# Optimization experiments

Hardware: AMD Instinct MI355X
Metric: run time of the kernel (lower is better)

The kernel has to match this reference:

```python
import jax, jax.numpy as jnp
import numpy as np
import math

B, S, E, H, D = 2, 2048, 1024, 16, 64  # batch, seq, embed, heads, head_dim


def setup_inputs() -> dict:
    key = jax.random.key(0)
    ks = jax.random.split(key, 10)
    scale = 1.0 / math.sqrt(D)
    return {
        "query": jax.random.normal(ks[0], (B, S, E), jnp.float32),
        "key": jax.random.normal(ks[1], (B, S, E), jnp.float32),
        "value": jax.random.normal(ks[2], (B, S, E), jnp.float32),
        "mask": jax.random.randint(ks[3], (1, 1, S, S), 0, 2, jnp.int32),
        # nn.Linear(single_dim, single_dim) weights (out,in) and biases
        "Wq": jax.random.uniform(ks[4], (D, D), jnp.float32, -scale, scale),
        "bq": jax.random.uniform(ks[5], (D,), jnp.float32, -scale, scale),
        "Wk": jax.random.uniform(ks[6], (D, D), jnp.float32, -scale, scale),
        "bk": jax.random.uniform(ks[7], (D,), jnp.float32, -scale, scale),
        "Wv": jax.random.uniform(ks[8], (D, D), jnp.float32, -scale, scale),
        "bv": jax.random.uniform(ks[9], (D,), jnp.float32, -scale, scale),
    }


def reference(query, key, value, mask, Wq, bq, Wk, bk, Wv, bv):
    b, sq, _ = query.shape
    sk = key.shape[1]
    # (b, s, E) -> (b, H, s, D)
    q = query.reshape(b, sq, H, D).transpose(0, 2, 1, 3)
    k = key.reshape(b, sk, H, D).transpose(0, 2, 1, 3)
    v = value.reshape(b, sk, H, D).transpose(0, 2, 1, 3)
    # per-head shared Linear on last dim: x @ W^T + b
    q = jnp.einsum('bhsd,ed->bhse', q, Wq) + bq
    k = jnp.einsum('bhsd,ed->bhse', k, Wk) + bk
    v = jnp.einsum('bhsd,ed->bhse', v, Wv) + bv
    scores = jnp.einsum('bhqd,bhkd->bhqk', q, k) / math.sqrt(D)
    scores = jnp.where(mask == 0, jnp.float32(-1e20), scores)
    attn = jax.nn.softmax(scores, axis=-1)
    out = jnp.einsum('bhqk,bhkd->bhqd', attn, v)
    return out.transpose(0, 2, 1, 3).reshape(b, sq, H * D)
```

## Files before the change

### kernel.cpp

```cpp
#include <hip/hip_runtime.h>

#define S_LEN 2048
#define E_DIM 1024
#define NH 16
#define HD 64
#define NT (S_LEN / 64)
#define SCALE_L2E 0.18033688011112042f

typedef __bf16 bf16;
typedef __attribute__((ext_vector_type(4))) bf16 bf16x4;
typedef __attribute__((ext_vector_type(8))) bf16 bf16x8;
typedef __attribute__((ext_vector_type(4))) float f32x4;
typedef unsigned long long u64;
typedef unsigned int u32;

#define MFMA(a, b, c) __builtin_amdgcn_mfma_f32_16x16x32_bf16((a), (b), (c), 0, 0, 0)

__device__ __forceinline__ bf16x8 cvt8(f32x4 a, f32x4 b) {
  bf16x8 r;
  r[0] = (bf16)a[0]; r[1] = (bf16)a[1]; r[2] = (bf16)a[2]; r[3] = (bf16)a[3];
  r[4] = (bf16)b[0]; r[5] = (bf16)b[1]; r[6] = (bf16)b[2]; r[7] = (bf16)b[3];
  return r;
}

__device__ __forceinline__ bf16x8 load_cvt_frag(const float* p) {
  f32x4 a = *(const f32x4*)(p);
  f32x4 b = *(const f32x4*)(p + 16);
  return cvt8(a, b);
}

__global__ __launch_bounds__(256) void kvproj_k(
    const float* __restrict__ Kin, const float* __restrict__ Vin,
    const float* __restrict__ Wk, const float* __restrict__ bk,
    const float* __restrict__ Wv, const float* __restrict__ bv,
    const int* __restrict__ mask,
    bf16* __restrict__ KpF, bf16* __restrict__ VpF, u64* __restrict__ bits) {
  const int xcd = blockIdx.x & 7;
  const int idx = blockIdx.x >> 3;
  const int bh = xcd * 4 + (idx >> 5);
  const int sblk = idx & 31;
  const int h = bh & (NH - 1);
  const int b = bh >> 4;
  const int lane = threadIdx.x & 63;
  const int wave = threadIdx.x >> 6;
  const int g = lane >> 4;
  const int c16 = lane & 15;
  const int sbase = sblk * 64 + wave * 16;
  const int srow = sbase + c16;

  const float* xk = Kin + ((size_t)b * S_LEN + srow) * E_DIM + h * HD;
  const float* xv = Vin + ((size_t)b * S_LEN + srow) * E_DIM + h * HD;
  bf16x8 xkf[2], xvf[2];
#pragma unroll
  for (int c = 0; c < 2; ++c) {
    xkf[c] = load_cvt_frag(xk + 32 * c + 4 * g);
    xvf[c] = load_cvt_frag(xv + 32 * c + 4 * g);
  }

#pragma unroll
  for (int nt = 0; nt < 4; ++nt) {
    const float* wr = Wk + (16 * nt + c16) * HD + 4 * g;
    f32x4 acc = {0.f, 0.f, 0.f, 0.f};
    acc = MFMA(xkf[0], load_cvt_frag(wr), acc);
    acc = MFMA(xkf[1], load_cvt_frag(wr + 32), acc);
    const float bias = bk[16 * nt + c16];
    const size_t fidx = (((size_t)bh * 32 + sblk) * 4 + wave) * 2 + (nt >> 1);
    const int e = (c16 & 3) + 4 * (nt & 1);
#pragma unroll
    for (int r = 0; r < 4; ++r) {
      const int lane_p = (c16 >> 2) * 16 + 4 * g + r;
      KpF[fidx * 512 + lane_p * 8 + e] = (bf16)(acc[r] + bias);
    }
  }
#pragma unroll
  for (int nt = 0; nt < 4; ++nt) {
    const float* wr = Wv + (16 * nt + c16) * HD + 4 * g;
    f32x4 acc = {0.f, 0.f, 0.f, 0.f};
    acc = MFMA(load_cvt_frag(wr), xvf[0], acc);
    acc = MFMA(load_cvt_frag(wr + 32), xvf[1], acc);
    const size_t fidx = (((size_t)bh * 32 + sblk) * 4 + nt) * 2 + (wave >> 1);
    const int e = (c16 & 3) + 4 * (wave & 1);
#pragma unroll
    for (int r = 0; r < 4; ++r) {
      const int dout = 16 * nt + 4 * g + r;
      const int lane_p = (c16 >> 2) * 16 + 4 * g + r;
      VpF[fidx * 512 + lane_p * 8 + e] = (bf16)(acc[r] + bv[dout]);
    }
  }

  const int wbase = blockIdx.x * 64 + wave * 16;
  int mv[16];
#pragma unroll
  for (int i = 0; i < 16; ++i) mv[i] = mask[(size_t)(wbase + i) * 64 + lane];
#pragma unroll
  for (int i = 0; i < 16; ++i) {
    const u64 bb = __ballot(mv[i] != 0);
    const int w = wbase + i;
    if (lane == 0) bits[(size_t)(w & 31) * S_LEN + (w >> 5)] = bb;
  }
}

__global__ __launch_bounds__(512) void attn_k(
    const float* __restrict__ Qin, const float* __restrict__ Wq, const float* __restrict__ bq,
    const bf16* __restrict__ KpF, const bf16* __restrict__ VpF,
    const u64* __restrict__ mbits, float* __restrict__ out) {
  const int xcd = blockIdx.x & 7;
  const int idx = blockIdx.x >> 3;
  const int bh = xcd * 4 + (idx >> 4);
  const int qc = idx & 15;
  const int h = bh & (NH - 1);
  const int b = bh >> 4;
  const int lane = threadIdx.x & 63;
  const int wave = threadIdx.x >> 6;
  const int g = lane >> 4;
  const int c16 = lane & 15;
  const int qrow = qc * 128 + wave * 16 + c16;

  __shared__ __align__(16) bf16 lds_kv[3][16 * 512];

  const float* xq = Qin + ((size_t)b * S_LEN + qrow) * E_DIM + h * HD;
  bf16x8 xqf[2];
#pragma unroll
  for (int c = 0; c < 2; ++c) xqf[c] = load_cvt_frag(xq + 32 * c + 4 * g);
  f32x4 qt[4];
#pragma unroll
  for (int t = 0; t < 4; ++t) {
    const float* wr = Wq + (16 * t + c16) * HD + 4 * g;
    f32x4 acc = {0.f, 0.f, 0.f, 0.f};
    acc = MFMA(load_cvt_frag(wr), xqf[0], acc);
    acc = MFMA(load_cvt_frag(wr + 32), xqf[1], acc);
#pragma unroll
    for (int r = 0; r < 4; ++r) acc[r] = (acc[r] + bq[16 * t + 4 * g + r]) * SCALE_L2E;
    qt[t] = acc;
  }
  bf16x8 qfrag0 = cvt8(qt[0], qt[1]);
  bf16x8 qfrag1 = cvt8(qt[2], qt[3]);

  bf16x8 ones;
#pragma unroll
  for (int i = 0; i < 8; ++i) ones[i] = (bf16)1.0f;

  const bf16* ktile = KpF + ((size_t)bh * 32) * 4096;
  const bf16* vtile = VpF + ((size_t)bh * 32) * 4096;
  const u64* mrowT = mbits + qrow;

  f32x4 o[4] = {};
  f32x4 o5 = {};

#define STAGE(BUF, T)                                                              \
  {                                                                                \
    const bf16* ks_ = ktile + (size_t)(T) * 4096 + wave * 512 + lane * 8;          \
    const bf16* vs_ = vtile + (size_t)(T) * 4096 + wave * 512 + lane * 8;          \
    __builtin_amdgcn_global_load_lds(                                              \
        (const __attribute__((address_space(1))) u32*)ks_,                         \
        (__attribute__((address_space(3))) u32*)((BUF) + wave * 512), 16, 0, 0);   \
    __builtin_amdgcn_global_load_lds(                                              \
        (const __attribute__((address_space(1))) u32*)vs_,                         \
        (__attribute__((address_space(3))) u32*)((BUF) + 4096 + wave * 512), 16, 0, 0); \
  }

  bf16* b0 = &lds_kv[0][0];
  bf16* b1 = &lds_kv[1][0];
  bf16* b2 = &lds_kv[2][0];

  u64 mca, mcb;

  STAGE(b0, 0)
  STAGE(b1, 1)
  mca = mrowT[0];
  mcb = mrowT[S_LEN];
  asm volatile("s_waitcnt vmcnt(4)" ::: "memory");
  asm volatile("s_barrier" ::: "memory");

#define ITER(BUF, NXT, MREG, T)                                                   \
  {                                                                               \
    const u64 mw_ = MREG;                                                         \
    const bool more_ = (T) + 2 < NT;                                              \
    if (more_) {                                                                  \
      MREG = mrowT[(size_t)((T) + 2) * S_LEN];                                    \
      STAGE(NXT, (T) + 2)                                                         \
    }                                                                             \
    bf16x8 kf[8], vfr[8];                                                         \
    _Pragma("unroll") for (int f = 0; f < 8; ++f)                                 \
        kf[f] = *(const bf16x8*)((BUF) + f * 512 + lane * 8);                     \
    f32x4 st[4];                                                                  \
    __builtin_amdgcn_s_setprio(1);                                                \
    _Pragma("unroll") for (int ks = 0; ks < 4; ++ks) {                            \
      f32x4 acc = {0.f, 0.f, 0.f, 0.f};                                           \
      acc = MFMA(kf[2 * ks], qfrag0, acc);                                        \
      acc = MFMA(kf[2 * ks + 1], qfrag1, acc);                                    \
      st[ks] = acc;                                                               \
    }                                                                             \
    __builtin_amdgcn_s_setprio(0);                                                \
    _Pragma("unroll") for (int f = 0; f < 8; ++f)                                 \
        vfr[f] = *(const bf16x8*)((BUF) + 4096 + f * 512 + lane * 8);             \
    const u64 mws = mw_ >> (4 * g);                                               \
    const u32 mlo = (u32)mws;                                                     \
    const u32 mhi = (u32)(mws >> 32);                                             \
    _Pragma("unroll") for (int ks = 0; ks < 4; ++ks) {                            \
      const u32 mword = (ks < 2) ? mlo : mhi;                                     \
      const int base = (ks & 1) * 16;                                             \
      _Pragma("unroll") for (int r = 0; r < 4; ++r) {                             \
        const float p = __builtin_amdgcn_exp2f(st[ks][r]);                        \
        const int keep = __builtin_amdgcn_sbfe(mword, base + r, 1);               \
        st[ks][r] = __uint_as_float(__float_as_uint(p) & (u32)keep);              \
      }                                                                           \
    }                                                                             \
    const bf16x8 pfrag0 = cvt8(st[0], st[1]);                                     \
    const bf16x8 pfrag1 = cvt8(st[2], st[3]);                                     \
    __builtin_amdgcn_s_setprio(1);                                                \
    _Pragma("unroll") for (int t = 0; t < 4; ++t) {                               \
      o[t] = MFMA(vfr[2 * t], pfrag0, o[t]);                                      \
      o[t] = MFMA(vfr[2 * t + 1], pfrag1, o[t]);                                  \
    }                                                                             \
    o5 = MFMA(ones, pfrag0, o5);                                                  \
    o5 = MFMA(ones, pfrag1, o5);                                                  \
    __builtin_amdgcn_s_setprio(0);                                                \
    if (more_) asm volatile("s_waitcnt vmcnt(3)" ::: "memory");                   \
    else       asm volatile("s_waitcnt vmcnt(0)" ::: "memory");                   \
    asm volatile("s_barrier" ::: "memory");                                       \
  }

  for (int t = 0; t < NT; t += 2) {
    ITER(b0, b2, mca, t)
    ITER(b1, b0, mcb, t + 1)
    bf16* tmp = b2; b2 = b1; b1 = b0; b0 = tmp;
  }
#undef ITER
#undef STAGE

  const float inv = 1.0f / o5[0];
  float* orow = out + ((size_t)b * S_LEN + qrow) * E_DIM + h * HD;
#pragma unroll
  for (int t = 0; t < 4; ++t) {
    f32x4 v;
#pragma unroll
    for (int r = 0; r < 4; ++r) v[r] = o[t][r] * inv;
    *(f32x4*)(orow + 16 * t + 4 * g) = v;
  }
}

extern "C" void kernel_launch(void* const* d_in, const int* in_sizes, int n_in,
                              void* d_out, int out_size, void* d_ws, size_t ws_size,
                              hipStream_t stream) {
  const float* Q = (const float*)d_in[0];
  const float* K = (const float*)d_in[1];
  const float* V = (const float*)d_in[2];
  const int* mask = (const int*)d_in[3];
  const float* Wq = (const float*)d_in[4];
  const float* bq = (const float*)d_in[5];
  const float* Wk = (const float*)d_in[6];
  const float* bk = (const float*)d_in[7];
  const float* Wv = (const float*)d_in[8];
  const float* bv = (const float*)d_in[9];
  float* out = (float*)d_out;

  char* ws = (char*)d_ws;
  const size_t proj_bytes = (size_t)2 * NH * S_LEN * HD * 2;
  bf16* KpF = (bf16*)ws;
  bf16* VpF = (bf16*)(ws + proj_bytes);
  u64* mbits = (u64*)(ws + 2 * proj_bytes);

  kvproj_k<<<2 * NH * (S_LEN / 64), 256, 0, stream>>>(K, V, Wk, bk, Wv, bv, mask,
                                                      KpF, VpF, mbits);
  attn_k<<<2 * NH * (S_LEN / 128), 512, 0, stream>>>(Q, Wq, bq, KpF, VpF, mbits, out);
}
```

Baseline: 87.97 us.

## Deepen K/V LDS pipeline to four buffers and prefetch next K fragments

The attention main loop now rotates through four LDS buffers instead of three, staging K/V tiles three iterations ahead. The mask words are kept in a 4-entry register ring. K fragments for the next tile are read from LDS into a second register set during the current iteration, and V fragments are loaded before the QK MFMAs. This is meant to hide global and LDS latency behind the MFMA work. In exchange it uses more LDS per block (64KB instead of 48KB) and more VGPRs, which may lower occupancy, and the wait counts must match the deeper prefetch.

```diff
diff --git a/kernel.cpp b/kernel.cpp
--- a/kernel.cpp
+++ b/kernel.cpp
@@ -116,7 +116,7 @@
   const int c16 = lane & 15;
   const int qrow = qc * 128 + wave * 16 + c16;
 
-  __shared__ __align__(16) bf16 lds_kv[3][16 * 512];
+  __shared__ __align__(16) bf16 lds_kv[4][16 * 512];
 
   const float* xq = Qin + ((size_t)b * S_LEN + qrow) * E_DIM + h * HD;
   bf16x8 xqf[2];
@@ -159,41 +159,46 @@
         (__attribute__((address_space(3))) u32*)((BUF) + 4096 + wave * 512), 16, 0, 0); \
   }
 
-  bf16* b0 = &lds_kv[0][0];
-  bf16* b1 = &lds_kv[1][0];
-  bf16* b2 = &lds_kv[2][0];
-
-  u64 mca, mcb;
-
-  STAGE(b0, 0)
-  STAGE(b1, 1)
-  mca = mrowT[0];
-  mcb = mrowT[S_LEN];
-  asm volatile("s_waitcnt vmcnt(4)" ::: "memory");
+  bf16* const B0 = &lds_kv[0][0];
+  bf16* const B1 = &lds_kv[1][0];
+  bf16* const B2 = &lds_kv[2][0];
+  bf16* const B3 = &lds_kv[3][0];
+
+  bf16x8 kfA[8], kfB[8], vfr[8];
+  u64 m4[4];
+
+  STAGE(B0, 0)
+  STAGE(B1, 1)
+  STAGE(B2, 2)
+  m4[0] = mrowT[0];
+  m4[1] = mrowT[S_LEN];
+  asm volatile("s_waitcnt vmcnt(1)" ::: "memory");
   asm volatile("s_barrier" ::: "memory");
-
-#define ITER(BUF, NXT, MREG, T)                                                   \
+#pragma unroll
+  for (int f = 0; f < 8; ++f) kfA[f] = *(const bf16x8*)(B0 + f * 512 + lane * 8);
+
+#define SLOT(BC, BN, BS, KFC, KFN, MK, T4)                                        \
   {                                                                               \
-    const u64 mw_ = MREG;                                                         \
-    const bool more_ = (T) + 2 < NT;                                              \
-    if (more_) {                                                                  \
-      MREG = mrowT[(size_t)((T) + 2) * S_LEN];                                    \
-      STAGE(NXT, (T) + 2)                                                         \
-    }                                                                             \
-    bf16x8 kf[8], vfr[8];                                                         \
+    const int t_ = (T4) + (MK);                                                   \
+    const u64 mw_ = m4[MK];                                                       \
+    if (t_ + 2 < NT) m4[((MK) + 2) & 3] = mrowT[(size_t)(t_ + 2) * S_LEN];        \
+    const bool more_ = (t_ + 3 < NT);                                             \
+    if (more_) STAGE(BS, t_ + 3)                                                  \
     _Pragma("unroll") for (int f = 0; f < 8; ++f)                                 \
-        kf[f] = *(const bf16x8*)((BUF) + f * 512 + lane * 8);                     \
+        vfr[f] = *(const bf16x8*)((BC) + 4096 + f * 512 + lane * 8);              \
+    if (t_ + 1 < NT) {                                                            \
+      _Pragma("unroll") for (int f = 0; f < 8; ++f)                               \
+          KFN[f] = *(const bf16x8*)((BN) + f * 512 + lane * 8);                   \
+    }                                                                             \
     f32x4 st[4];                                                                  \
     __builtin_amdgcn_s_setprio(1);                                                \
     _Pragma("unroll") for (int ks = 0; ks < 4; ++ks) {                            \
       f32x4 acc = {0.f, 0.f, 0.f, 0.f};                                           \
-      acc = MFMA(kf[2 * ks], qfrag0, acc);                                        \
-      acc = MFMA(kf[2 * ks + 1], qfrag1, acc);                                    \
+      acc = MFMA(KFC[2 * ks], qfrag0, acc);                                       \
+      acc = MFMA(KFC[2 * ks + 1], qfrag1, acc);                                   \
       st[ks] = acc;                                                               \
     }                                                                             \
     __builtin_amdgcn_s_setprio(0);                                                \
-    _Pragma("unroll") for (int f = 0; f < 8; ++f)                                 \
-        vfr[f] = *(const bf16x8*)((BUF) + 4096 + f * 512 + lane * 8);             \
     const u64 mws = mw_ >> (4 * g);                                               \
     const u32 mlo = (u32)mws;                                                     \
     const u32 mhi = (u32)(mws >> 32);                                             \
@@ -221,12 +226,13 @@
     asm volatile("s_barrier" ::: "memory");                                       \
   }
 
-  for (int t = 0; t < NT; t += 2) {
-    ITER(b0, b2, mca, t)
-    ITER(b1, b0, mcb, t + 1)
-    bf16* tmp = b2; b2 = b1; b1 = b0; b0 = tmp;
-  }
-#undef ITER
+  for (int t4 = 0; t4 < NT; t4 += 4) {
+    SLOT(B0, B1, B3, kfA, kfB, 0, t4)
+    SLOT(B1, B2, B0, kfB, kfA, 1, t4)
+    SLOT(B2, B3, B1, kfA, kfB, 2, t4)
+    SLOT(B3, B0, B2, kfB, kfA, 3, t4)
+  }
+#undef SLOT
 #undef STAGE
 
   const float inv = 1.0f / o5[0];
```

After: 101.6 us. 1.16x slower.
